# Performance work log

Measured on AMD Instinct MI355X. Metric: run time of the kernel, lower is better.

## Reference

```python
import jax, jax.numpy as jnp
import numpy as np

EPS = 1e-5
TEMPERATURE = 1.0

def _finger_masks():
    # (5, 21) anatomical hyperedge masks: fingers cover node indices 1..20 in groups of 4
    m = np.zeros((5, 21), np.float32)
    for i in range(5):
        m[i, 1 + 4 * i: 5 + 4 * i] = 1.0
    return jnp.asarray(m)

def setup_inputs() -> dict:
    key = jax.random.key(0)
    ks = jax.random.split(key, 13)
    N, C, T, V, E = 128, 128, 256, 21, 8
    return {
        "x": jax.random.normal(ks[0], (N, C, T, V), jnp.float32),
        "dyn_w": jax.random.normal(ks[1], (E, C), jnp.float32) * 0.05,
        "dyn_b": jax.random.normal(ks[2], (E,), jnp.float32) * 0.05,
        "dyn_gamma": jax.random.uniform(ks[3], (E,), jnp.float32, 0.5, 1.5),
        "dyn_beta": jax.random.normal(ks[4], (E,), jnp.float32) * 0.05,
        "dyn_mean": jax.random.normal(ks[5], (E,), jnp.float32) * 0.05,
        "dyn_var": jax.random.uniform(ks[6], (E,), jnp.float32, 0.5, 1.5),
        "ft_w": jax.random.normal(ks[7], (C, C), jnp.float32) * 0.05,
        "ft_b": jax.random.normal(ks[8], (C,), jnp.float32) * 0.05,
        "ft_gamma": jax.random.uniform(ks[9], (C,), jnp.float32, 0.5, 1.5),
        "ft_beta": jax.random.normal(ks[10], (C,), jnp.float32) * 0.05,
        "ft_mean": jax.random.normal(ks[11], (C,), jnp.float32) * 0.05,
        "ft_var": jax.random.uniform(ks[12], (C,), jnp.float32, 0.5, 1.5),
    }

def reference(x, dyn_w, dyn_b, dyn_gamma, dyn_beta, dyn_mean, dyn_var,
              ft_w, ft_b, ft_gamma, ft_beta, ft_mean, ft_var):
    N = x.shape[0]
    # dynamic hyperedge generation: mean over T -> conv1x1 -> BN -> ReLU -> softmax over V
    xm = x.mean(axis=2)                                         # (N, C, V)
    h = jnp.einsum('ncv,ec->nev', xm, dyn_w) + dyn_b[None, :, None]
    scale = dyn_gamma * jax.lax.rsqrt(dyn_var + EPS)
    h = (h - dyn_mean[None, :, None]) * scale[None, :, None] + dyn_beta[None, :, None]
    h = jax.nn.relu(h)
    H_dyn = jax.nn.softmax(h / TEMPERATURE, axis=-1)            # (N, E, V)
    H_phy = jnp.broadcast_to(_finger_masks()[None], (N, 5, 21))
    H = jnp.concatenate([H_dyn, H_phy], axis=1)                 # (N, M=E+5, V)
    # feature transform: conv1x1 -> BN -> ReLU
    xf = jnp.einsum('nctv,oc->notv', x, ft_w) + ft_b[None, :, None, None]
    fscale = ft_gamma * jax.lax.rsqrt(ft_var + EPS)
    xf = (xf - ft_mean[None, :, None, None]) * fscale[None, :, None, None] + ft_beta[None, :, None, None]
    xf = jax.nn.relu(xf)                                        # (N, Cout, T, V)
    # hypergraph message passing: node -> edge -> node
    Y = jnp.einsum('nmv,nctv->ncmt', H, xf)                     # (N, Cout, M, T)
    Xr = jnp.einsum('nmv,ncmt->nctv', H, Y)                     # (N, Cout, T, V)
    return Xr + x  # residual (in_channels == out_channels)
```

## Files before the change

### kernel.cpp

```cpp
#include <hip/hip_runtime.h>
#include <hip/hip_bf16.h>
#include <math.h>

#define EPS 1e-5f

static constexpr int N_ = 128, C_ = 128, T_ = 256, V_ = 21, E_ = 8, M_ = 13;
static constexpr int TV_ = T_ * V_;
static constexpr int NT_ = 4;
static constexpr int ST_ = NT_ * V_;
static constexpr int SROWS = 96;
static constexpr int XF_PITCH = 48;
static constexpr int LDS_BYTES = SROWS * 256 + 64;

#define SWZ(s)  (((((s) & 7) ^ ((((s) >> 3) & 3) << 1))) << 4)
#define EXOR(r) ((((r) >> 5) & 3) << 4)

typedef short bf16x8 __attribute__((ext_vector_type(8)));
typedef short s16x4  __attribute__((ext_vector_type(4)));
typedef float f32x4  __attribute__((ext_vector_type(4)));

__device__ inline short f2bf(float v) {
    __hip_bfloat16 b = __float2bfloat16(v);
    return *reinterpret_cast<short*>(&b);
}

__global__ __launch_bounds__(256) void prep_kernel(
    const float* __restrict__ ft_w, const float* __restrict__ ft_b,
    const float* __restrict__ ft_gamma, const float* __restrict__ ft_beta,
    const float* __restrict__ ft_mean, const float* __restrict__ ft_var,
    __hip_bfloat16* __restrict__ w_bf, float* __restrict__ sc_g, float* __restrict__ sh_g)
{
    int tid = blockIdx.x * 256 + threadIdx.x;
    if (tid < C_ * C_) w_bf[tid] = __float2bfloat16(ft_w[tid]);
    if (tid < C_) {
        float sc = ft_gamma[tid] * rsqrtf(ft_var[tid] + EPS);
        sc_g[tid] = sc;
        sh_g[tid] = (ft_b[tid] - ft_mean[tid]) * sc + ft_beta[tid];
    }
}

__global__ __launch_bounds__(256) void mean_kernel(const float* __restrict__ x,
                                                   float* __restrict__ xm) {
    __shared__ float slab[TV_];
    __shared__ float partial[V_ * 8];
    const int nc = blockIdx.x;
    const int tid = threadIdx.x;
    const float4* src4 = (const float4*)(x + (size_t)nc * TV_);
    float4* slab4 = (float4*)slab;
    #pragma unroll
    for (int it = 0; it < 6; ++it) {
        int idx = it * 256 + tid;
        if (idx < TV_ / 4) slab4[idx] = src4[idx];
    }
    __syncthreads();
    if (tid < V_ * 8) {
        int v = tid >> 3, g = tid & 7;
        float s = 0.f;
        #pragma unroll
        for (int tt = 0; tt < 32; ++tt) s += slab[(g * 32 + tt) * V_ + v];
        partial[v * 8 + g] = s;
    }
    __syncthreads();
    if (tid < V_) {
        float s = 0.f;
        #pragma unroll
        for (int g = 0; g < 8; ++g) s += partial[tid * 8 + g];
        xm[(size_t)nc * V_ + tid] = s * (1.0f / T_);
    }
}

__global__ __launch_bounds__(64) void hyper_kernel(
    const float* __restrict__ xm, const float* __restrict__ dyn_w,
    const float* __restrict__ dyn_b,
    const float* __restrict__ dyn_gamma, const float* __restrict__ dyn_beta,
    const float* __restrict__ dyn_mean, const float* __restrict__ dyn_var,
    __hip_bfloat16* __restrict__ A_bf)
{
    __shared__ float xs[C_ * V_];
    __shared__ float Hs[M_ * V_];
    const int n = blockIdx.x;
    const int l = threadIdx.x;
    const float* src = xm + (size_t)n * C_ * V_;
    for (int idx = l; idx < C_ * V_; idx += 64) xs[idx] = src[idx];
    __syncthreads();
    for (int idx = l; idx < E_ * V_; idx += 64) {
        int e = idx / V_, v = idx - e * V_;
        float acc = 0.f;
        for (int c = 0; c < C_; ++c) acc = fmaf(xs[c * V_ + v], dyn_w[e * C_ + c], acc);
        acc += dyn_b[e];
        float scale = dyn_gamma[e] * rsqrtf(dyn_var[e] + EPS);
        acc = (acc - dyn_mean[e]) * scale + dyn_beta[e];
        Hs[idx] = fmaxf(acc, 0.f);
    }
    __syncthreads();
    if (l < E_) {
        float row[V_];
        float mx = -1e30f;
        #pragma unroll
        for (int v = 0; v < V_; ++v) { row[v] = Hs[l * V_ + v]; mx = fmaxf(mx, row[v]); }
        float s = 0.f;
        #pragma unroll
        for (int v = 0; v < V_; ++v) { row[v] = __expf(row[v] - mx); s += row[v]; }
        float inv = 1.0f / s;
        #pragma unroll
        for (int v = 0; v < V_; ++v) Hs[l * V_ + v] = row[v] * inv;
    } else if (l < M_) {
        int i = l - E_;
        #pragma unroll
        for (int v = 0; v < V_; ++v)
            Hs[l * V_ + v] = (v >= 1 + 4 * i && v < 5 + 4 * i) ? 1.0f : 0.0f;
    }
    __syncthreads();
    for (int idx = l; idx < 32 * 32; idx += 64) {
        int u = idx >> 5, v = idx & 31;
        float s = 0.f;
        if (u < V_ && v < V_) {
            #pragma unroll
            for (int m = 0; m < M_; ++m) s = fmaf(Hs[m * V_ + u], Hs[m * V_ + v], s);
        }
        A_bf[(size_t)n * 1024 + idx] = __float2bfloat16(s);
    }
}

__global__ __launch_bounds__(512, 8) void main_kernel(
    const float* __restrict__ x, const __hip_bfloat16* __restrict__ w_bf,
    const float* __restrict__ sc_g, const float* __restrict__ sh_g,
    const __hip_bfloat16* __restrict__ A_bf, float* __restrict__ out)
{
    __shared__ __align__(16) char lds[LDS_BYTES];
    __shared__ float sc_s[C_], sh_s[C_];

    const int st = blockIdx.x;
    const int n  = blockIdx.y;
    const int tid = threadIdx.x;
    const int w = tid >> 6;
    const int l = tid & 63;
    const int hi = l >> 4;
    const int lo = l & 15;
    const int s0 = st * ST_;
    const size_t xbase = (size_t)n * C_ * TV_ + s0;

    if (tid < C_) { sc_s[tid] = sc_g[tid]; sh_s[tid] = sh_g[tid]; }

    const int o_row = 16 * w + lo;
    bf16x8 wf[4];
    #pragma unroll
    for (int kk = 0; kk < 4; ++kk)
        wf[kk] = *(const bf16x8*)((const short*)w_bf + o_row * C_ + kk * 32 + 8 * hi);

    const short* Abf_n = (const short*)A_bf + (size_t)n * 1024;
    const bf16x8 bA0 = *(const bf16x8*)(Abf_n + lo * 32 + 8 * hi);
    const bf16x8 bA1 = *(const bf16x8*)(Abf_n + (16 + lo) * 32 + 8 * hi);

    auto stage_one = [&](int idx) {
        int cg = idx / 21, q = idx - cg * 21;
        int c0 = cg * 4, sq = q * 4;
        f32x4 f[4];
        #pragma unroll
        for (int i = 0; i < 4; ++i)
            f[i] = *(const f32x4*)(x + xbase + (size_t)(c0 + i) * TV_ + sq);
        #pragma unroll
        for (int i = 0; i < 4; ++i) {
            int s = sq + i;
            s16x4 pk;
            #pragma unroll
            for (int j = 0; j < 4; ++j) pk[j] = f2bf(f[j][i]);
            int byte = (s * 256 + c0 * 2) ^ SWZ(s);
            *(s16x4*)(lds + byte) = pk;
        }
    };
    stage_one(tid);
    if (tid < 672 - 512) stage_one(tid + 512);

    if (tid < 384) {
        int srow = ST_ + (tid >> 5);
        int k = tid & 31;
        int byte = (srow * 256 + k * 8) ^ SWZ(srow);
        *(unsigned long long*)(lds + byte) = 0ull;
    }
    __syncthreads();

    f32x4 acc[6];
    #pragma unroll
    for (int nf = 0; nf < 6; ++nf) acc[nf] = (f32x4){0.f, 0.f, 0.f, 0.f};
    #pragma unroll
    for (int kk = 0; kk < 4; ++kk) {
        #pragma unroll
        for (int nf = 0; nf < 6; ++nf) {
            int srow = 16 * nf + lo;
            int byte = (srow * 256 + (kk * 32 + 8 * hi) * 2) ^ SWZ(srow);
            bf16x8 b = *(const bf16x8*)(lds + byte);
            acc[nf] = __builtin_amdgcn_mfma_f32_16x16x32_bf16(wf[kk], b, acc[nf], 0, 0, 0);
        }
    }
    __syncthreads();

    const int obase = 16 * w + 4 * hi;
    float scr[4], shr[4];
    #pragma unroll
    for (int r = 0; r < 4; ++r) { scr[r] = sc_s[obase + r]; shr[r] = sh_s[obase + r]; }
    #pragma unroll
    for (int nf = 0; nf < 6; ++nf) {
        int s = 16 * nf + lo;
        if (s < ST_) {
            int t = s / V_, u = s - t * V_;
            #pragma unroll
            for (int r = 0; r < 4; ++r) {
                float vv = fmaxf(fmaf(acc[nf][r], scr[r], shr[r]), 0.f);
                int row = (obase + r) * NT_ + t;
                *(short*)(lds + ((row * XF_PITCH + u * 2) ^ EXOR(row))) = f2bf(vv);
            }
        }
    }
    {
        int row = tid;
        int e = EXOR(row);
        *(short*)(lds + ((row * XF_PITCH + 42) ^ e)) = 0;
        *(int*)(lds + ((row * XF_PITCH + 44) ^ e)) = 0;
    }
    if (tid < 16) *(int*)(lds + SROWS * 256 + tid * 4) = 0;
    __syncthreads();

    bf16x8 xfr[4];
    #pragma unroll
    for (int i = 0; i < 4; ++i) {
        int row = 16 * (4 * w + i) + lo;
        xfr[i] = *(const bf16x8*)(lds + ((row * XF_PITCH + 16 * hi) ^ EXOR(row)));
    }
    #pragma unroll
    for (int i = 0; i < 4; ++i) {
        f32x4 d0 = (f32x4){0.f, 0.f, 0.f, 0.f};
        f32x4 d1 = (f32x4){0.f, 0.f, 0.f, 0.f};
        d0 = __builtin_amdgcn_mfma_f32_16x16x32_bf16(xfr[i], bA0, d0, 0, 0, 0);
        d1 = __builtin_amdgcn_mfma_f32_16x16x32_bf16(xfr[i], bA1, d1, 0, 0, 0);
        int row0 = 16 * (4 * w + i) + 4 * hi;
        #pragma unroll
        for (int r = 0; r < 4; ++r) {
            int row = row0 + r;
            int o = row >> 2, t = row & 3;
            size_t g = xbase + (size_t)o * TV_ + t * V_;
            out[g + lo] = d0[r] + x[g + lo];
            if (lo < V_ - 16) out[g + 16 + lo] = d1[r] + x[g + 16 + lo];
        }
    }
}

extern "C" void kernel_launch(void* const* d_in, const int* in_sizes, int n_in,
                              void* d_out, int out_size, void* d_ws, size_t ws_size,
                              hipStream_t stream) {
    const float* x         = (const float*)d_in[0];
    const float* dyn_w     = (const float*)d_in[1];
    const float* dyn_b     = (const float*)d_in[2];
    const float* dyn_gamma = (const float*)d_in[3];
    const float* dyn_beta  = (const float*)d_in[4];
    const float* dyn_mean  = (const float*)d_in[5];
    const float* dyn_var   = (const float*)d_in[6];
    const float* ft_w      = (const float*)d_in[7];
    const float* ft_b      = (const float*)d_in[8];
    const float* ft_gamma  = (const float*)d_in[9];
    const float* ft_beta   = (const float*)d_in[10];
    const float* ft_mean   = (const float*)d_in[11];
    const float* ft_var    = (const float*)d_in[12];
    float* out = (float*)d_out;

    char* ws = (char*)d_ws;
    float* xm  = (float*)ws;                                   ws += (size_t)N_ * C_ * V_ * 4;
    __hip_bfloat16* A_bf = (__hip_bfloat16*)ws;                ws += (size_t)N_ * 1024 * 2;
    __hip_bfloat16* w_bf = (__hip_bfloat16*)ws;                ws += (size_t)C_ * C_ * 2;
    float* sc_g = (float*)ws;                                  ws += C_ * 4;
    float* sh_g = (float*)ws;                                  ws += C_ * 4;

    prep_kernel<<<64, 256, 0, stream>>>(ft_w, ft_b, ft_gamma, ft_beta, ft_mean, ft_var,
                                        w_bf, sc_g, sh_g);
    mean_kernel<<<N_ * C_, 256, 0, stream>>>(x, xm);
    hyper_kernel<<<N_, 64, 0, stream>>>(xm, dyn_w, dyn_b, dyn_gamma, dyn_beta,
                                        dyn_mean, dyn_var, A_bf);
    main_kernel<<<dim3(T_ / NT_, N_), 512, 0, stream>>>(x, w_bf, sc_g, sh_g, A_bf, out);
}
```

Measured before the change: 414.4 us.

## Process four time sub-tiles per block with double-buffered LDS and register prefetch

Each block now loops over four consecutive 4-timestep sub-tiles instead of one. The next sub-tile's x data is loaded into registers during the current tile's MFMA work and written to an alternate LDS buffer, which overlaps global-load latency with compute. Per-block setup (weight fragments, the per-sample A matrix, BN scale/shift) is amortised over four tiles, and the grid shrinks fourfold. In exchange LDS per block roughly doubles and the occupancy hint drops from 8 to 4. The explicit zeroing of the xf padding bytes is also dropped, so the second MFMA now reads leftover staged data where those bytes used to be zero; the matching A entries are zero, so this is harmless only while that data stays finite.

```diff
diff --git a/kernel.cpp b/kernel.cpp
--- a/kernel.cpp
+++ b/kernel.cpp
@@ -8,9 +8,10 @@
 static constexpr int TV_ = T_ * V_;
 static constexpr int NT_ = 4;
 static constexpr int ST_ = NT_ * V_;
-static constexpr int SROWS = 96;
+static constexpr int NSUB = 4;
+static constexpr int BT_ = NT_ * NSUB;
+static constexpr int SBUF = 96 * 256;
 static constexpr int XF_PITCH = 48;
-static constexpr int LDS_BYTES = SROWS * 256 + 64;
 
 #define SWZ(s)  (((((s) & 7) ^ ((((s) >> 3) & 3) << 1))) << 4)
 #define EXOR(r) ((((r) >> 5) & 3) << 4)
@@ -122,25 +123,26 @@
     }
 }
 
-__global__ __launch_bounds__(512, 8) void main_kernel(
+__global__ __launch_bounds__(512, 4) void main_kernel(
     const float* __restrict__ x, const __hip_bfloat16* __restrict__ w_bf,
     const float* __restrict__ sc_g, const float* __restrict__ sh_g,
     const __hip_bfloat16* __restrict__ A_bf, float* __restrict__ out)
 {
-    __shared__ __align__(16) char lds[LDS_BYTES];
+    __shared__ __align__(16) char lds[2 * SBUF + 64];
     __shared__ float sc_s[C_], sh_s[C_];
 
-    const int st = blockIdx.x;
+    const int gt = blockIdx.x;
     const int n  = blockIdx.y;
     const int tid = threadIdx.x;
     const int w = tid >> 6;
     const int l = tid & 63;
     const int hi = l >> 4;
     const int lo = l & 15;
-    const int s0 = st * ST_;
-    const size_t xbase = (size_t)n * C_ * TV_ + s0;
+    const int t0 = gt * BT_;
+    const size_t xn = (size_t)n * C_ * TV_;
 
     if (tid < C_) { sc_s[tid] = sc_g[tid]; sh_s[tid] = sh_g[tid]; }
+    if (tid < 16) *(int*)(lds + 2 * SBUF + tid * 4) = 0;
 
     const int o_row = 16 * w + lo;
     bf16x8 wf[4];
@@ -152,95 +154,115 @@
     const bf16x8 bA0 = *(const bf16x8*)(Abf_n + lo * 32 + 8 * hi);
     const bf16x8 bA1 = *(const bf16x8*)(Abf_n + (16 + lo) * 32 + 8 * hi);
 
-    auto stage_one = [&](int idx) {
-        int cg = idx / 21, q = idx - cg * 21;
-        int c0 = cg * 4, sq = q * 4;
-        f32x4 f[4];
+    const int cg0 = tid / 21,          q0 = tid - cg0 * 21;
+    const int cg1 = (tid + 512) / 21,  q1 = (tid + 512) - cg1 * 21;
+    const int c00 = cg0 * 4, sq0 = q0 * 4;
+    const int c01 = cg1 * 4, sq1 = q1 * 4;
+    const bool has2 = (tid < 672 - 512);
+
+    f32x4 pf[8];
+
+    auto issue_loads = [&](int it) {
+        const float* src = x + xn + (size_t)(t0 + it * NT_) * V_;
         #pragma unroll
         for (int i = 0; i < 4; ++i)
-            f[i] = *(const f32x4*)(x + xbase + (size_t)(c0 + i) * TV_ + sq);
+            pf[i] = *(const f32x4*)(src + (size_t)(c00 + i) * TV_ + sq0);
+        if (has2) {
+            #pragma unroll
+            for (int i = 0; i < 4; ++i)
+                pf[4 + i] = *(const f32x4*)(src + (size_t)(c01 + i) * TV_ + sq1);
+        }
+    };
+    auto write_stage = [&](char* buf) {
         #pragma unroll
         for (int i = 0; i < 4; ++i) {
-            int s = sq + i;
-            s16x4 pk;
-            #pragma unroll
-            for (int j = 0; j < 4; ++j) pk[j] = f2bf(f[j][i]);
-            int byte = (s * 256 + c0 * 2) ^ SWZ(s);
-            *(s16x4*)(lds + byte) = pk;
+            int s = sq0 + i;
+            s16x4 pk = { f2bf(pf[0][i]), f2bf(pf[1][i]), f2bf(pf[2][i]), f2bf(pf[3][i]) };
+            *(s16x4*)(buf + ((s * 256 + c00 * 2) ^ SWZ(s))) = pk;
+        }
+        if (has2) {
+            #pragma unroll
+            for (int i = 0; i < 4; ++i) {
+                int s = sq1 + i;
+                s16x4 pk = { f2bf(pf[4][i]), f2bf(pf[5][i]), f2bf(pf[6][i]), f2bf(pf[7][i]) };
+                *(s16x4*)(buf + ((s * 256 + c01 * 2) ^ SWZ(s))) = pk;
+            }
+        }
+        if (tid < 384) {
+            int srow = ST_ + (tid >> 5);
+            int k8 = (tid & 31) * 8;
+            *(unsigned long long*)(buf + ((srow * 256 + k8) ^ SWZ(srow))) = 0ull;
         }
     };
-    stage_one(tid);
-    if (tid < 672 - 512) stage_one(tid + 512);
-
-    if (tid < 384) {
-        int srow = ST_ + (tid >> 5);
-        int k = tid & 31;
-        int byte = (srow * 256 + k * 8) ^ SWZ(srow);
-        *(unsigned long long*)(lds + byte) = 0ull;
-    }
-    __syncthreads();
-
-    f32x4 acc[6];
-    #pragma unroll
-    for (int nf = 0; nf < 6; ++nf) acc[nf] = (f32x4){0.f, 0.f, 0.f, 0.f};
-    #pragma unroll
-    for (int kk = 0; kk < 4; ++kk) {
-        #pragma unroll
-        for (int nf = 0; nf < 6; ++nf) {
-            int srow = 16 * nf + lo;
-            int byte = (srow * 256 + (kk * 32 + 8 * hi) * 2) ^ SWZ(srow);
-            bf16x8 b = *(const bf16x8*)(lds + byte);
-            acc[nf] = __builtin_amdgcn_mfma_f32_16x16x32_bf16(wf[kk], b, acc[nf], 0, 0, 0);
-        }
-    }
+
+    issue_loads(0);
+    write_stage(lds);
     __syncthreads();
 
     const int obase = 16 * w + 4 * hi;
     float scr[4], shr[4];
     #pragma unroll
     for (int r = 0; r < 4; ++r) { scr[r] = sc_s[obase + r]; shr[r] = sh_s[obase + r]; }
+
     #pragma unroll
-    for (int nf = 0; nf < 6; ++nf) {
-        int s = 16 * nf + lo;
-        if (s < ST_) {
-            int t = s / V_, u = s - t * V_;
+    for (int it = 0; it < NSUB; ++it) {
+        char* Scur = lds + (it & 1) * SBUF;
+        char* Snxt = lds + ((it & 1) ^ 1) * SBUF;
+
+        if (it < NSUB - 1) issue_loads(it + 1);
+
+        f32x4 acc[6];
+        #pragma unroll
+        for (int nf = 0; nf < 6; ++nf) acc[nf] = (f32x4){0.f, 0.f, 0.f, 0.f};
+        #pragma unroll
+        for (int kk = 0; kk < 4; ++kk) {
+            #pragma unroll
+            for (int nf = 0; nf < 6; ++nf) {
+                int srow = 16 * nf + lo;
+                int byte = (srow * 256 + (kk * 32 + 8 * hi) * 2) ^ SWZ(srow);
+                bf16x8 b = *(const bf16x8*)(Scur + byte);
+                acc[nf] = __builtin_amdgcn_mfma_f32_16x16x32_bf16(wf[kk], b, acc[nf], 0, 0, 0);
+            }
+        }
+        __syncthreads();
+
+        #pragma unroll
+        for (int nf = 0; nf < 6; ++nf) {
+            int s = 16 * nf + lo;
+            if (s < ST_) {
+                int t = s / V_, u = s - t * V_;
+                #pragma unroll
+                for (int r = 0; r < 4; ++r) {
+                    float vv = fmaxf(fmaf(acc[nf][r], scr[r], shr[r]), 0.f);
+                    int row = (obase + r) * NT_ + t;
+                    *(short*)(Scur + ((row * XF_PITCH + u * 2) ^ EXOR(row))) = f2bf(vv);
+                }
+            }
+        }
+        if (it < NSUB - 1) write_stage(Snxt);
+        __syncthreads();
+
+        bf16x8 xfr[4];
+        #pragma unroll
+        for (int i = 0; i < 4; ++i) {
+            int row = 16 * (4 * w + i) + lo;
+            xfr[i] = *(const bf16x8*)(Scur + ((row * XF_PITCH + 16 * hi) ^ EXOR(row)));
+        }
+        #pragma unroll
+        for (int i = 0; i < 4; ++i) {
+            f32x4 d0 = (f32x4){0.f, 0.f, 0.f, 0.f};
+            f32x4 d1 = (f32x4){0.f, 0.f, 0.f, 0.f};
+            d0 = __builtin_amdgcn_mfma_f32_16x16x32_bf16(xfr[i], bA0, d0, 0, 0, 0);
+            d1 = __builtin_amdgcn_mfma_f32_16x16x32_bf16(xfr[i], bA1, d1, 0, 0, 0);
+            int row0 = 16 * (4 * w + i) + 4 * hi;
             #pragma unroll
             for (int r = 0; r < 4; ++r) {
-                float vv = fmaxf(fmaf(acc[nf][r], scr[r], shr[r]), 0.f);
-                int row = (obase + r) * NT_ + t;
-                *(short*)(lds + ((row * XF_PITCH + u * 2) ^ EXOR(row))) = f2bf(vv);
+                int row = row0 + r;
+                int o = row >> 2, tl = row & 3;
+                size_t g = xn + (size_t)o * TV_ + (size_t)(t0 + it * NT_ + tl) * V_;
+                out[g + lo] = d0[r] + x[g + lo];
+                if (lo < V_ - 16) out[g + 16 + lo] = d1[r] + x[g + 16 + lo];
             }
-        }
-    }
-    {
-        int row = tid;
-        int e = EXOR(row);
-        *(short*)(lds + ((row * XF_PITCH + 42) ^ e)) = 0;
-        *(int*)(lds + ((row * XF_PITCH + 44) ^ e)) = 0;
-    }
-    if (tid < 16) *(int*)(lds + SROWS * 256 + tid * 4) = 0;
-    __syncthreads();
-
-    bf16x8 xfr[4];
-    #pragma unroll
-    for (int i = 0; i < 4; ++i) {
-        int row = 16 * (4 * w + i) + lo;
-        xfr[i] = *(const bf16x8*)(lds + ((row * XF_PITCH + 16 * hi) ^ EXOR(row)));
-    }
-    #pragma unroll
-    for (int i = 0; i < 4; ++i) {
-        f32x4 d0 = (f32x4){0.f, 0.f, 0.f, 0.f};
-        f32x4 d1 = (f32x4){0.f, 0.f, 0.f, 0.f};
-        d0 = __builtin_amdgcn_mfma_f32_16x16x32_bf16(xfr[i], bA0, d0, 0, 0, 0);
-        d1 = __builtin_amdgcn_mfma_f32_16x16x32_bf16(xfr[i], bA1, d1, 0, 0, 0);
-        int row0 = 16 * (4 * w + i) + 4 * hi;
-        #pragma unroll
-        for (int r = 0; r < 4; ++r) {
-            int row = row0 + r;
-            int o = row >> 2, t = row & 3;
-            size_t g = xbase + (size_t)o * TV_ + t * V_;
-            out[g + lo] = d0[r] + x[g + lo];
-            if (lo < V_ - 16) out[g + 16 + lo] = d1[r] + x[g + 16 + lo];
         }
     }
 }
@@ -275,5 +297,5 @@
     mean_kernel<<<N_ * C_, 256, 0, stream>>>(x, xm);
     hyper_kernel<<<N_, 64, 0, stream>>>(xm, dyn_w, dyn_b, dyn_gamma, dyn_beta,
                                         dyn_mean, dyn_var, A_bf);
-    main_kernel<<<dim3(T_ / NT_, N_), 512, 0, stream>>>(x, w_bf, sc_g, sh_g, A_bf, out);
-}
+    main_kernel<<<dim3(T_ / BT_, N_), 512, 0, stream>>>(x, w_bf, sc_g, sh_g, A_bf, out);
+}
```

New measurement: 598.7 us. 44.5% more time.
